# Optimization experiments

Measured on AMD Instinct MI355X. Metric: run time of the kernel, lower is better.

Reference implementation:

```python
import jax, jax.numpy as jnp
import numpy as np

N, E = 10000, 160000
IN_C, HID, K = 128, 256, 16


def setup_inputs() -> dict:
    key = jax.random.key(0)
    ks = jax.random.split(key, 8)
    x = jax.random.normal(ks[0], (N, IN_C), jnp.float32)
    edge_index = jax.random.randint(ks[1], (2, E), 0, N, dtype=jnp.int32).astype(jnp.int64)
    edge_attributes = jax.random.uniform(ks[2], (E,), jnp.float32)
    W1 = jax.random.normal(ks[3], (IN_C, HID), jnp.float32) / np.sqrt(IN_C)
    b1 = jnp.zeros((HID,), jnp.float32)
    W2 = jax.random.normal(ks[4], (HID, HID), jnp.float32) / np.sqrt(HID)
    b2 = jnp.zeros((HID,), jnp.float32)
    Wp = jax.random.normal(ks[5], (HID, K), jnp.float32) / np.sqrt(HID)
    bp = jnp.zeros((K,), jnp.float32)
    return dict(x=x, edge_index=edge_index, edge_attributes=edge_attributes,
                W1=W1, b1=b1, W2=W2, b2=b2, Wp=Wp, bp=bp)


def _gcn_conv(x, src, dst, ew, W, b):
    """GCNConv with add_self_loops=True, normalize=True, edge weights."""
    n = x.shape[0]
    loop = jnp.arange(n)
    s = jnp.concatenate([src, loop])
    d = jnp.concatenate([dst, loop])
    w = jnp.concatenate([ew, jnp.ones((n,), x.dtype)])
    deg = jax.ops.segment_sum(w, d, num_segments=n)           # weighted in-degree
    dis = jnp.where(deg > 0, jax.lax.rsqrt(deg), 0.0)         # D^{-1/2}, inf -> 0
    norm = dis[s] * w * dis[d]                                # per-edge coefficient
    h = x @ W                                                 # transform first
    msg = norm[:, None] * h[s]                                # gather from source
    out = jax.ops.segment_sum(msg, d, num_segments=n)         # scatter-add to target
    return out + b


def reference(x, edge_index, edge_attributes, W1, b1, W2, b2, Wp, bp):
    src, dst = edge_index[0], edge_index[1]
    ew = edge_attributes
    h = jax.nn.relu(_gcn_conv(x, src, dst, ew, W1, b1))
    h = jax.nn.relu(_gcn_conv(h, src, dst, ew, W2, b2))

    # to_dense_adj (duplicate edges accumulate)
    adj = jnp.zeros((N, N), h.dtype).at[src, dst].add(ew)

    # DMoNPooling (dropout=0, eval): s = softmax(Linear(h))
    s = jax.nn.softmax(h @ Wp + bp, axis=-1)                  # [N, K]

    out_adj = s.T @ adj @ s                                   # [K, K]
    deg = adj.sum(axis=1)                                     # [N]
    m = deg.sum() / 2
    ca = s.T @ deg[:, None]                                   # [K, 1]
    cb = deg[None, :] @ s                                     # [1, K]
    normalizer = (ca @ cb) / (2 * m)
    spectral_loss = -jnp.trace(out_adj - normalizer) / (2 * m)

    cluster_size = s.sum(axis=0)                              # [K]
    cluster_loss = jnp.linalg.norm(cluster_size) / N * jnp.sqrt(jnp.float32(K)) - 1.0

    loss = 100.0 * (spectral_loss + cluster_loss)
    # PyG returns s with a leading batch dim of 1
    return s[None], loss, 100.0 * spectral_loss, 100.0 * cluster_loss
```

## Files before the change

### kernel.cpp

```cpp
#include <hip/hip_runtime.h>
#include <math.h>


#define ER_BLOCKS 128

__device__ __forceinline__ bool ei_is_i64(const int* __restrict__ ei) {
  return ((ei[1] | ei[3] | ei[5] | ei[7]) == 0);
}
__device__ __forceinline__ int ld_idx(const int* __restrict__ ei, int pos, bool i64) {
  return i64 ? ei[2 * pos] : ei[pos];
}

__global__ __launch_bounds__(256) void zero_init(int4* __restrict__ p, int n4) {
  int i = blockIdx.x * 256 + threadIdx.x;
  if (i < n4) p[i] = make_int4(0, 0, 0, 0);
}

__global__ __launch_bounds__(256) void edge_count(const int* __restrict__ ei,
                                                  const float* __restrict__ ew,
                                                  int* __restrict__ cnt,
                                                  float* __restrict__ deg, int E) {
  int e = blockIdx.x * 256 + threadIdx.x;
  if (e >= E) return;
  bool i64 = ei_is_i64(ei);
  int d = ld_idx(ei, E + e, i64);
  atomicAdd(&cnt[d], 1);
  atomicAdd(&deg[d], ew[e]);
}

__global__ __launch_bounds__(1024) void scan_kernel(const int* __restrict__ cnt,
                                                    int* __restrict__ rowptr, int n) {
  __shared__ int sums[1024];
  int tid = threadIdx.x;
  int CH = (n + 1023) >> 10;
  int beg = tid * CH, end = min(beg + CH, n);
  int s = 0;
  for (int i = beg; i < end; ++i) s += cnt[i];
  sums[tid] = s;
  __syncthreads();
  for (int off = 1; off < 1024; off <<= 1) {
    int v = (tid >= off) ? sums[tid - off] : 0;
    __syncthreads();
    sums[tid] += v;
    __syncthreads();
  }
  int run = (tid == 0) ? 0 : sums[tid - 1];
  for (int i = beg; i < end; ++i) { rowptr[i] = run; run += cnt[i]; }
  if (tid == 1023) rowptr[n] = run;
}

__global__ __launch_bounds__(256) void scatter_edges(const int* __restrict__ ei,
                                                     const float* __restrict__ ew,
                                                     const int* __restrict__ rowptr,
                                                     int* __restrict__ cur,
                                                     const float* __restrict__ deg,
                                                     int* __restrict__ col,
                                                     float* __restrict__ coef, int E) {
  int e = blockIdx.x * 256 + threadIdx.x;
  if (e >= E) return;
  bool i64 = ei_is_i64(ei);
  int s = ld_idx(ei, e, i64);
  int d = ld_idx(ei, E + e, i64);
  int p = rowptr[d] + atomicAdd(&cur[d], 1);
  col[p] = s;
  float ds = 1.0f / sqrtf(deg[s] + 1.0f);
  float dd = 1.0f / sqrtf(deg[d] + 1.0f);
  coef[p] = ds * ew[e] * dd;
}

template <int CH>
__global__ __launch_bounds__(256) void aggregate_pre(const float* __restrict__ src,
                                                     const int* __restrict__ rowptr,
                                                     const int* __restrict__ col,
                                                     const float* __restrict__ coef,
                                                     const float* __restrict__ deg,
                                                     float* __restrict__ out, int N) {
  constexpr int Q = CH / 4;
  constexpr int NS = 256 / Q;
  int i = blockIdx.x;
  int t = threadIdx.x;
  int q = t % Q, slot = t / Q;
  int e0 = rowptr[i], e1 = rowptr[i + 1];
  float4 acc = make_float4(0.f, 0.f, 0.f, 0.f);
  for (int p = e0 + slot; p < e1; p += NS) {
    int c = col[p];
    float w = coef[p];
    float4 v = *reinterpret_cast<const float4*>(&src[(size_t)c * CH + q * 4]);
    acc.x += w * v.x; acc.y += w * v.y; acc.z += w * v.z; acc.w += w * v.w;
  }
  __shared__ float4 red[256];
  red[t] = acc;
  __syncthreads();
  if (slot == 0) {
#pragma unroll
    for (int s2 = 1; s2 < NS; ++s2) {
      float4 o = red[s2 * Q + q];
      acc.x += o.x; acc.y += o.y; acc.z += o.z; acc.w += o.w;
    }
    float w0 = 1.0f / (deg[i] + 1.0f);
    float4 xv = *reinterpret_cast<const float4*>(&src[(size_t)i * CH + q * 4]);
    acc.x += w0 * xv.x; acc.y += w0 * xv.y; acc.z += w0 * xv.z; acc.w += w0 * xv.w;
    *reinterpret_cast<float4*>(&out[(size_t)i * CH + q * 4]) = acc;
  }
}

__global__ __launch_bounds__(256) void gemm_bias_act(const float* __restrict__ A,
                                                     const float* __restrict__ B,
                                                     const float* __restrict__ bias,
                                                     float* __restrict__ C,
                                                     int M, int K, int N, int relu) {
  __shared__ float As[32][68];
  __shared__ float Bs[32][64];
  int tid = threadIdx.x;
  int tx = tid & 15, ty = tid >> 4;
  int row0 = blockIdx.x * 64, col0 = blockIdx.y * 64;
  float acc[4][4] = {};
  for (int k0 = 0; k0 < K; k0 += 32) {
#pragma unroll
    for (int r = 0; r < 2; ++r) {
      int lin = (tid + r * 256) * 4;
      int ar = lin >> 5, ak = lin & 31;
      float4 av = make_float4(0.f, 0.f, 0.f, 0.f);
      int grow = row0 + ar;
      if (grow < M) av = *reinterpret_cast<const float4*>(&A[(size_t)grow * K + k0 + ak]);
      As[ak + 0][ar] = av.x; As[ak + 1][ar] = av.y;
      As[ak + 2][ar] = av.z; As[ak + 3][ar] = av.w;
      int bk = lin >> 6, bn = lin & 63;
      float4 bv = *reinterpret_cast<const float4*>(&B[(size_t)(k0 + bk) * N + col0 + bn]);
      *reinterpret_cast<float4*>(&Bs[bk][bn]) = bv;
    }
    __syncthreads();
#pragma unroll
    for (int k = 0; k < 32; ++k) {
      float4 av = *reinterpret_cast<const float4*>(&As[k][ty * 4]);
      float4 bv = *reinterpret_cast<const float4*>(&Bs[k][tx * 4]);
      float a[4] = {av.x, av.y, av.z, av.w};
      float b[4] = {bv.x, bv.y, bv.z, bv.w};
#pragma unroll
      for (int i = 0; i < 4; ++i)
#pragma unroll
        for (int j = 0; j < 4; ++j) acc[i][j] += a[i] * b[j];
    }
    __syncthreads();
  }
  float4 bb = *reinterpret_cast<const float4*>(&bias[col0 + tx * 4]);
  float bias4[4] = {bb.x, bb.y, bb.z, bb.w};
#pragma unroll
  for (int i = 0; i < 4; ++i) {
    int gr = row0 + ty * 4 + i;
    if (gr < M) {
      float o[4];
#pragma unroll
      for (int j = 0; j < 4; ++j) {
        float v = acc[i][j] + bias4[j];
        o[j] = relu ? fmaxf(v, 0.0f) : v;
      }
      *reinterpret_cast<float4*>(&C[(size_t)gr * N + col0 + tx * 4]) =
          make_float4(o[0], o[1], o[2], o[3]);
    }
  }
}

__global__ __launch_bounds__(256) void pool_kernel(const float* __restrict__ h,
                                                   const float* __restrict__ Wp,
                                                   const float* __restrict__ bp,
                                                   float* __restrict__ s_out,
                                                   float* __restrict__ cs_part, int N) {
  __shared__ float Wps[256 * 16];
  __shared__ float cs_loc[16];
  int tid = threadIdx.x;
  for (int idx = tid; idx < 4096; idx += 256) Wps[idx] = Wp[idx];
  if (tid < 16) cs_loc[tid] = 0.f;
  __syncthreads();
  int lane = tid & 63;
  int wave = tid >> 6;
  int k = lane & 15, g = lane >> 4;
  int node = blockIdx.x * 16 + wave * 4 + g;
  float acc = 0.f;
  if (node < N) {
    const float4* hrow = reinterpret_cast<const float4*>(h + (size_t)node * 256);
#pragma unroll 8
    for (int c4 = 0; c4 < 64; ++c4) {
      float4 hv = hrow[c4];
      int cb = c4 * 4;
      acc += hv.x * Wps[(cb + 0) * 16 + k];
      acc += hv.y * Wps[(cb + 1) * 16 + k];
      acc += hv.z * Wps[(cb + 2) * 16 + k];
      acc += hv.w * Wps[(cb + 3) * 16 + k];
    }
    acc += bp[k];
  }
  float mx = acc;
#pragma unroll
  for (int off = 1; off < 16; off <<= 1) mx = fmaxf(mx, __shfl_xor(mx, off));
  float ex = (node < N) ? expf(acc - mx) : 0.f;
  float sm = ex;
#pragma unroll
  for (int off = 1; off < 16; off <<= 1) sm += __shfl_xor(sm, off);
  float sval = (node < N) ? ex / sm : 0.f;
  if (node < N) s_out[(size_t)node * 16 + k] = sval;
  float v = sval;
  v += __shfl_xor(v, 16);
  v += __shfl_xor(v, 32);
  if (lane < 16) atomicAdd(&cs_loc[lane], v);
  __syncthreads();
  if (tid < 16) cs_part[(size_t)blockIdx.x * 16 + tid] = cs_loc[tid];
}

__global__ __launch_bounds__(256) void edge_reduce(const int* __restrict__ ei,
                                                   const float* __restrict__ ew,
                                                   const float* __restrict__ s,
                                                   float* __restrict__ part, int E) {
  __shared__ float loc[18];
  int tid = threadIdx.x;
  if (tid < 18) loc[tid] = 0.f;
  __syncthreads();
  bool i64 = ei_is_i64(ei);
  float dot = 0.f, w = 0.f;
  float ca[16];
#pragma unroll
  for (int k = 0; k < 16; ++k) ca[k] = 0.f;
  for (int e = blockIdx.x * 256 + tid; e < E; e += gridDim.x * 256) {
    int a = ld_idx(ei, e, i64);
    int b = ld_idx(ei, E + e, i64);
    float we = ew[e];
    const float4* sa = reinterpret_cast<const float4*>(s + (size_t)a * 16);
    const float4* sb = reinterpret_cast<const float4*>(s + (size_t)b * 16);
    float d = 0.f;
#pragma unroll
    for (int q = 0; q < 4; ++q) {
      float4 av = sa[q], bv = sb[q];
      d += av.x * bv.x + av.y * bv.y + av.z * bv.z + av.w * bv.w;
      ca[q * 4 + 0] += we * av.x; ca[q * 4 + 1] += we * av.y;
      ca[q * 4 + 2] += we * av.z; ca[q * 4 + 3] += we * av.w;
    }
    dot += we * d;
    w += we;
  }
#pragma unroll
  for (int off = 32; off; off >>= 1) {
    dot += __shfl_xor(dot, off);
    w += __shfl_xor(w, off);
#pragma unroll
    for (int k = 0; k < 16; ++k) ca[k] += __shfl_xor(ca[k], off);
  }
  if ((tid & 63) == 0) {
    atomicAdd(&loc[0], dot);
    atomicAdd(&loc[1], w);
#pragma unroll
    for (int k = 0; k < 16; ++k) atomicAdd(&loc[2 + k], ca[k]);
  }
  __syncthreads();
  if (tid < 18) part[(size_t)blockIdx.x * 18 + tid] = loc[tid];
}

__global__ __launch_bounds__(256) void finalize(const float* __restrict__ epart,
                                                const float* __restrict__ cs_part,
                                                int pool_blocks,
                                                float* __restrict__ out,
                                                int N, int s_elems) {
  __shared__ float red[18];
  __shared__ float csl[256];
  __shared__ float cs[16];
  int tid = threadIdx.x;
  if (tid < 18) {
    float a = 0.f;
    for (int b = 0; b < ER_BLOCKS; ++b) a += epart[(size_t)b * 18 + tid];
    red[tid] = a;
  }
  {
    int k = tid & 15, sl = tid >> 4;
    float a = 0.f;
    for (int b = sl; b < pool_blocks; b += 16) a += cs_part[(size_t)b * 16 + k];
    csl[tid] = a;
  }
  __syncthreads();
  if (tid < 16) {
    float a = 0.f;
#pragma unroll
    for (int sl = 0; sl < 16; ++sl) a += csl[sl * 16 + tid];
    cs[tid] = a;
  }
  __syncthreads();
  if (tid == 0) {
    float tr = red[0], m2 = red[1];
    float ca2 = 0.f, cs2 = 0.f;
    for (int k = 0; k < 16; ++k) {
      ca2 += red[2 + k] * red[2 + k];
      cs2 += cs[k] * cs[k];
    }
    float sp = -(tr - ca2 / m2) / m2;
    float cl = sqrtf(cs2) / (float)N * 4.0f - 1.0f;
    out[s_elems + 0] = 100.f * (sp + cl);
    out[s_elems + 1] = 100.f * sp;
    out[s_elems + 2] = 100.f * cl;
  }
}

extern "C" void kernel_launch(void* const* d_in, const int* in_sizes, int n_in,
                              void* d_out, int out_size, void* d_ws, size_t ws_size,
                              hipStream_t stream) {
  const float* x  = (const float*)d_in[0];
  const int*   ei = (const int*)d_in[1];
  const float* ew = (const float*)d_in[2];
  const float* W1 = (const float*)d_in[3];
  const float* b1 = (const float*)d_in[4];
  const float* W2 = (const float*)d_in[5];
  const float* b2 = (const float*)d_in[6];
  const float* Wp = (const float*)d_in[7];
  const float* bp = (const float*)d_in[8];
  float* out = (float*)d_out;

  const int IN_C = 128, HID = 256;
  const int N = in_sizes[0] / IN_C;
  const int E = in_sizes[2];
  const int pool_blocks = (N + 15) / 16;

  char* p = (char*)d_ws;
  auto alloc = [&](size_t b) { char* r = p; p += (b + 255) & ~(size_t)255; return r; };
  float* deg     = (float*)alloc((size_t)N * 4);
  int*   cnt     = (int*)alloc((size_t)N * 4);
  int*   cur     = (int*)alloc((size_t)N * 4);
  char*  zero_end = p;
  float* ax      = (float*)alloc((size_t)N * IN_C * 4);
  float* h       = (float*)alloc((size_t)N * HID * 4);
  float* ah      = (float*)alloc((size_t)N * HID * 4);
  float* h2      = (float*)alloc((size_t)N * HID * 4);
  int*   rowptr  = (int*)alloc((size_t)(N + 1) * 4);
  int*   col     = (int*)alloc((size_t)E * 4);
  float* coef    = (float*)alloc((size_t)E * 4);
  float* epart   = (float*)alloc((size_t)ER_BLOCKS * 18 * 4);
  float* cs_part = (float*)alloc((size_t)pool_blocks * 16 * 4);
  if ((size_t)(p - (char*)d_ws) > ws_size) return;

  int zn4 = (int)((zero_end - (char*)deg) >> 4);
  zero_init<<<(zn4 + 255) / 256, 256, 0, stream>>>((int4*)deg, zn4);

  int eb = (E + 255) / 256;
  edge_count<<<eb, 256, 0, stream>>>(ei, ew, cnt, deg, E);
  scan_kernel<<<1, 1024, 0, stream>>>(cnt, rowptr, N);
  scatter_edges<<<eb, 256, 0, stream>>>(ei, ew, rowptr, cur, deg, col, coef, E);

  aggregate_pre<128><<<N, 256, 0, stream>>>(x, rowptr, col, coef, deg, ax, N);
  dim3 gg((N + 63) / 64, HID / 64);
  gemm_bias_act<<<gg, 256, 0, stream>>>(ax, W1, b1, h, N, IN_C, HID, 1);
  aggregate_pre<256><<<N, 256, 0, stream>>>(h, rowptr, col, coef, deg, ah, N);
  gemm_bias_act<<<gg, 256, 0, stream>>>(ah, W2, b2, h2, N, HID, HID, 1);

  pool_kernel<<<pool_blocks, 256, 0, stream>>>(h2, Wp, bp, out, cs_part, N);
  edge_reduce<<<ER_BLOCKS, 256, 0, stream>>>(ei, ew, out, epart, E);
  finalize<<<1, 256, 0, stream>>>(epart, cs_part, pool_blocks, out, N, N * 16);
}
```

Before: 166.8 us.

## Use split-bf16 MFMA GEMMs with aggregation emitting hi/lo bf16 operands

Replaces the FP32 SIMT tiled GEMM with an MFMA 16x16x32 bf16 kernel. Accuracy is kept close to FP32 by splitting each operand into high and low bf16 parts and summing three products (hi*hi, lo*hi, hi*lo). The aggregation kernels now write the hi/lo bf16 pair directly, and a new kernel transposes and splits the weights each call. This aims to move GEMM work onto matrix cores, at the cost of an extra launch and triple MFMA work.

```diff
diff --git a/kernel.cpp b/kernel.cpp
--- a/kernel.cpp
+++ b/kernel.cpp
@@ -3,6 +3,20 @@
 
 
 #define ER_BLOCKS 128
+
+typedef unsigned short u16;
+typedef __attribute__((ext_vector_type(8))) short short8v;
+typedef __attribute__((ext_vector_type(4))) float float4v;
+typedef __attribute__((ext_vector_type(4))) unsigned short ushort4v;
+
+__device__ __forceinline__ u16 f2bf_rne(float x) {
+  unsigned u = __float_as_uint(x);
+  u = (u + 0x7fffu + ((u >> 16) & 1u)) >> 16;
+  return (u16)u;
+}
+__device__ __forceinline__ float bf2f(u16 h) {
+  return __uint_as_float(((unsigned)h) << 16);
+}
 
 __device__ __forceinline__ bool ei_is_i64(const int* __restrict__ ei) {
   return ((ei[1] | ei[3] | ei[5] | ei[7]) == 0);
@@ -14,6 +28,29 @@
 __global__ __launch_bounds__(256) void zero_init(int4* __restrict__ p, int n4) {
   int i = blockIdx.x * 256 + threadIdx.x;
   if (i < n4) p[i] = make_int4(0, 0, 0, 0);
+}
+
+__global__ __launch_bounds__(256) void conv_weights(const float* __restrict__ W1,
+                                                    const float* __restrict__ W2,
+                                                    u16* __restrict__ w1hi, u16* __restrict__ w1lo,
+                                                    u16* __restrict__ w2hi, u16* __restrict__ w2lo) {
+  const int T1 = 256 * 128;
+  const int T2 = 256 * 256;
+  int t = blockIdx.x * 256 + threadIdx.x;
+  if (t < T1) {
+    int n = t >> 7, k = t & 127;
+    float x = W1[k * 256 + n];
+    u16 h = f2bf_rne(x);
+    w1hi[t] = h;
+    w1lo[t] = f2bf_rne(x - bf2f(h));
+  } else if (t < T1 + T2) {
+    int t2 = t - T1;
+    int n = t2 >> 8, k = t2 & 255;
+    float x = W2[k * 256 + n];
+    u16 h = f2bf_rne(x);
+    w2hi[t2] = h;
+    w2lo[t2] = f2bf_rne(x - bf2f(h));
+  }
 }
 
 __global__ __launch_bounds__(256) void edge_count(const int* __restrict__ ei,
@@ -74,7 +111,8 @@
                                                      const int* __restrict__ col,
                                                      const float* __restrict__ coef,
                                                      const float* __restrict__ deg,
-                                                     float* __restrict__ out, int N) {
+                                                     u16* __restrict__ ohi,
+                                                     u16* __restrict__ olo, int N) {
   constexpr int Q = CH / 4;
   constexpr int NS = 256 / Q;
   int i = blockIdx.x;
@@ -100,63 +138,96 @@
     float w0 = 1.0f / (deg[i] + 1.0f);
     float4 xv = *reinterpret_cast<const float4*>(&src[(size_t)i * CH + q * 4]);
     acc.x += w0 * xv.x; acc.y += w0 * xv.y; acc.z += w0 * xv.z; acc.w += w0 * xv.w;
-    *reinterpret_cast<float4*>(&out[(size_t)i * CH + q * 4]) = acc;
-  }
-}
-
-__global__ __launch_bounds__(256) void gemm_bias_act(const float* __restrict__ A,
-                                                     const float* __restrict__ B,
-                                                     const float* __restrict__ bias,
-                                                     float* __restrict__ C,
-                                                     int M, int K, int N, int relu) {
-  __shared__ float As[32][68];
-  __shared__ float Bs[32][64];
+    float a[4] = {acc.x, acc.y, acc.z, acc.w};
+    ushort4v hv, lv;
+#pragma unroll
+    for (int j = 0; j < 4; ++j) {
+      u16 h = f2bf_rne(a[j]);
+      hv[j] = h;
+      lv[j] = f2bf_rne(a[j] - bf2f(h));
+    }
+    *reinterpret_cast<ushort4v*>(&ohi[(size_t)i * CH + q * 4]) = hv;
+    *reinterpret_cast<ushort4v*>(&olo[(size_t)i * CH + q * 4]) = lv;
+  }
+}
+
+__global__ __launch_bounds__(256) void gemm_mfma(const u16* __restrict__ Ahi,
+                                                 const u16* __restrict__ Alo,
+                                                 const u16* __restrict__ Wthi,
+                                                 const u16* __restrict__ Wtlo,
+                                                 const float* __restrict__ bias,
+                                                 float* __restrict__ C,
+                                                 int M, int K) {
+  __shared__ u16 As_hi[64][40], As_lo[64][40];
+  __shared__ u16 Bs_hi[64][40], Bs_lo[64][40];
   int tid = threadIdx.x;
-  int tx = tid & 15, ty = tid >> 4;
+  int w = tid >> 6, l = tid & 63;
+  int wm = w >> 1, wn = w & 1;
   int row0 = blockIdx.x * 64, col0 = blockIdx.y * 64;
-  float acc[4][4] = {};
+  int srow = tid >> 2, sc = (tid & 3) * 8;
+  int fr = l & 15, kg = (l >> 4) * 8;
+
+  float4v acc[2][2];
+#pragma unroll
+  for (int i = 0; i < 2; ++i)
+#pragma unroll
+    for (int j = 0; j < 2; ++j) acc[i][j] = (float4v){0.f, 0.f, 0.f, 0.f};
+
   for (int k0 = 0; k0 < K; k0 += 32) {
-#pragma unroll
-    for (int r = 0; r < 2; ++r) {
-      int lin = (tid + r * 256) * 4;
-      int ar = lin >> 5, ak = lin & 31;
-      float4 av = make_float4(0.f, 0.f, 0.f, 0.f);
-      int grow = row0 + ar;
-      if (grow < M) av = *reinterpret_cast<const float4*>(&A[(size_t)grow * K + k0 + ak]);
-      As[ak + 0][ar] = av.x; As[ak + 1][ar] = av.y;
-      As[ak + 2][ar] = av.z; As[ak + 3][ar] = av.w;
-      int bk = lin >> 6, bn = lin & 63;
-      float4 bv = *reinterpret_cast<const float4*>(&B[(size_t)(k0 + bk) * N + col0 + bn]);
-      *reinterpret_cast<float4*>(&Bs[bk][bn]) = bv;
+    {
+      int gr = row0 + srow;
+      uint4 zero = make_uint4(0, 0, 0, 0);
+      uint4 vh = zero, vl = zero;
+      if (gr < M) {
+        vh = *reinterpret_cast<const uint4*>(&Ahi[(size_t)gr * K + k0 + sc]);
+        vl = *reinterpret_cast<const uint4*>(&Alo[(size_t)gr * K + k0 + sc]);
+      }
+      *reinterpret_cast<uint4*>(&As_hi[srow][sc]) = vh;
+      *reinterpret_cast<uint4*>(&As_lo[srow][sc]) = vl;
+      int bn = col0 + srow;
+      uint4 bh = *reinterpret_cast<const uint4*>(&Wthi[(size_t)bn * K + k0 + sc]);
+      uint4 bl = *reinterpret_cast<const uint4*>(&Wtlo[(size_t)bn * K + k0 + sc]);
+      *reinterpret_cast<uint4*>(&Bs_hi[srow][sc]) = bh;
+      *reinterpret_cast<uint4*>(&Bs_lo[srow][sc]) = bl;
     }
     __syncthreads();
-#pragma unroll
-    for (int k = 0; k < 32; ++k) {
-      float4 av = *reinterpret_cast<const float4*>(&As[k][ty * 4]);
-      float4 bv = *reinterpret_cast<const float4*>(&Bs[k][tx * 4]);
-      float a[4] = {av.x, av.y, av.z, av.w};
-      float b[4] = {bv.x, bv.y, bv.z, bv.w};
-#pragma unroll
-      for (int i = 0; i < 4; ++i)
-#pragma unroll
-        for (int j = 0; j < 4; ++j) acc[i][j] += a[i] * b[j];
-    }
+    short8v ah[2], al[2], bh[2], bl[2];
+#pragma unroll
+    for (int i = 0; i < 2; ++i) {
+      int r = wm * 32 + i * 16 + fr;
+      ah[i] = *reinterpret_cast<const short8v*>(&As_hi[r][kg]);
+      al[i] = *reinterpret_cast<const short8v*>(&As_lo[r][kg]);
+    }
+#pragma unroll
+    for (int j = 0; j < 2; ++j) {
+      int n = wn * 32 + j * 16 + fr;
+      bh[j] = *reinterpret_cast<const short8v*>(&Bs_hi[n][kg]);
+      bl[j] = *reinterpret_cast<const short8v*>(&Bs_lo[n][kg]);
+    }
+#pragma unroll
+    for (int i = 0; i < 2; ++i)
+#pragma unroll
+      for (int j = 0; j < 2; ++j) {
+        acc[i][j] = __builtin_amdgcn_mfma_f32_16x16x32_bf16(ah[i], bh[j], acc[i][j], 0, 0, 0);
+        acc[i][j] = __builtin_amdgcn_mfma_f32_16x16x32_bf16(al[i], bh[j], acc[i][j], 0, 0, 0);
+        acc[i][j] = __builtin_amdgcn_mfma_f32_16x16x32_bf16(ah[i], bl[j], acc[i][j], 0, 0, 0);
+      }
     __syncthreads();
   }
-  float4 bb = *reinterpret_cast<const float4*>(&bias[col0 + tx * 4]);
-  float bias4[4] = {bb.x, bb.y, bb.z, bb.w};
-#pragma unroll
-  for (int i = 0; i < 4; ++i) {
-    int gr = row0 + ty * 4 + i;
-    if (gr < M) {
-      float o[4];
-#pragma unroll
-      for (int j = 0; j < 4; ++j) {
-        float v = acc[i][j] + bias4[j];
-        o[j] = relu ? fmaxf(v, 0.0f) : v;
+#pragma unroll
+  for (int j = 0; j < 2; ++j) {
+    int gc = col0 + wn * 32 + j * 16 + fr;
+    float bj = bias[gc];
+#pragma unroll
+    for (int i = 0; i < 2; ++i) {
+#pragma unroll
+      for (int r = 0; r < 4; ++r) {
+        int gr = row0 + wm * 32 + i * 16 + (l >> 4) * 4 + r;
+        if (gr < M) {
+          float v = acc[i][j][r] + bj;
+          C[(size_t)gr * 256 + gc] = fmaxf(v, 0.0f);
+        }
       }
-      *reinterpret_cast<float4*>(&C[(size_t)gr * N + col0 + tx * 4]) =
-          make_float4(o[0], o[1], o[2], o[3]);
     }
   }
 }
@@ -322,10 +393,16 @@
   int*   cnt     = (int*)alloc((size_t)N * 4);
   int*   cur     = (int*)alloc((size_t)N * 4);
   char*  zero_end = p;
-  float* ax      = (float*)alloc((size_t)N * IN_C * 4);
+  u16*   axhi    = (u16*)alloc((size_t)N * IN_C * 2);
+  u16*   axlo    = (u16*)alloc((size_t)N * IN_C * 2);
+  u16*   ahhi    = (u16*)alloc((size_t)N * HID * 2);
+  u16*   ahlo    = (u16*)alloc((size_t)N * HID * 2);
   float* h       = (float*)alloc((size_t)N * HID * 4);
-  float* ah      = (float*)alloc((size_t)N * HID * 4);
   float* h2      = (float*)alloc((size_t)N * HID * 4);
+  u16*   w1hi    = (u16*)alloc((size_t)256 * 128 * 2);
+  u16*   w1lo    = (u16*)alloc((size_t)256 * 128 * 2);
+  u16*   w2hi    = (u16*)alloc((size_t)256 * 256 * 2);
+  u16*   w2lo    = (u16*)alloc((size_t)256 * 256 * 2);
   int*   rowptr  = (int*)alloc((size_t)(N + 1) * 4);
   int*   col     = (int*)alloc((size_t)E * 4);
   float* coef    = (float*)alloc((size_t)E * 4);
@@ -335,17 +412,19 @@
 
   int zn4 = (int)((zero_end - (char*)deg) >> 4);
   zero_init<<<(zn4 + 255) / 256, 256, 0, stream>>>((int4*)deg, zn4);
+  conv_weights<<<(256 * 128 + 256 * 256 + 255) / 256, 256, 0, stream>>>(
+      W1, W2, w1hi, w1lo, w2hi, w2lo);
 
   int eb = (E + 255) / 256;
   edge_count<<<eb, 256, 0, stream>>>(ei, ew, cnt, deg, E);
   scan_kernel<<<1, 1024, 0, stream>>>(cnt, rowptr, N);
   scatter_edges<<<eb, 256, 0, stream>>>(ei, ew, rowptr, cur, deg, col, coef, E);
 
-  aggregate_pre<128><<<N, 256, 0, stream>>>(x, rowptr, col, coef, deg, ax, N);
   dim3 gg((N + 63) / 64, HID / 64);
-  gemm_bias_act<<<gg, 256, 0, stream>>>(ax, W1, b1, h, N, IN_C, HID, 1);
-  aggregate_pre<256><<<N, 256, 0, stream>>>(h, rowptr, col, coef, deg, ah, N);
-  gemm_bias_act<<<gg, 256, 0, stream>>>(ah, W2, b2, h2, N, HID, HID, 1);
+  aggregate_pre<128><<<N, 256, 0, stream>>>(x, rowptr, col, coef, deg, axhi, axlo, N);
+  gemm_mfma<<<gg, 256, 0, stream>>>(axhi, axlo, w1hi, w1lo, b1, h, N, IN_C);
+  aggregate_pre<256><<<N, 256, 0, stream>>>(h, rowptr, col, coef, deg, ahhi, ahlo, N);
+  gemm_mfma<<<gg, 256, 0, stream>>>(ahhi, ahlo, w2hi, w2lo, b2, h2, N, HID);
 
   pool_kernel<<<pool_blocks, 256, 0, stream>>>(h2, Wp, bp, out, cs_part, N);
   edge_reduce<<<ER_BLOCKS, 256, 0, stream>>>(ei, ew, out, epart, E);
```

New measurement: 153.7 us. -7.8%, faster.
